# Performance work log

Measured on AMD Instinct MI355X. Metric: run time of the kernel, lower is better.

Reference implementation:

```python
import jax, jax.numpy as jnp
import numpy as np

N, K, DIM = 50000, 16, 256
SLOPE = 0.2

def _leaky(x):
    return jnp.where(x >= 0, x, SLOPE * x)

def _mlp(x, w, b):
    # torch nn.Linear followed by LeakyReLU(0.2); w is [in, out]
    return _leaky(x @ w + b)

def setup_inputs() -> dict:
    key = jax.random.key(0)
    ks = jax.random.split(key, 14)
    d4, d2 = DIM // 4, DIM // 2
    def lin(k, i, o):
        kw, kb = jax.random.split(k)
        s = 1.0 / np.sqrt(i)
        return (jax.random.uniform(kw, (i, o), jnp.float32, -s, s),
                jax.random.uniform(kb, (o,), jnp.float32, -s, s))
    w_res, b_res = lin(ks[0], DIM, DIM)
    w_init, b_init = lin(ks[1], DIM, d4)
    w_g1, b_g1 = lin(ks[2], 4, d4)
    w_g2, b_g2 = lin(ks[3], 4, d2)
    w_fin, b_fin = lin(ks[4], DIM, DIM)
    return {
        "input_features": jax.random.normal(ks[5], (N, DIM), jnp.float32),
        "geom_features": jax.random.normal(ks[6], (N, K, 4), jnp.float32),
        "closest_indices": jax.random.randint(ks[7], (N, K), 0, N, jnp.int32),
        "w_res": w_res, "b_res": b_res,
        "w_init": w_init, "b_init": b_init,
        "w_g1": w_g1, "b_g1": b_g1,
        "w_g2": w_g2, "b_g2": b_g2,
        "w_fin": w_fin, "b_fin": b_fin,
    }

def _lfa(feat, geom, idx, w_g, b_g):
    # feat: [N, d]; geom: [N, K, 4]; idx: [N, K]
    g = _mlp(geom, w_g, b_g)                 # [N, K, d]
    gathered = feat[idx]                      # [N, K, d] gather over points
    combined = jnp.concatenate([g, gathered], axis=-1)  # [N, K, 2d]
    return jnp.mean(combined, axis=1)         # [N, 2d]

def reference(input_features, geom_features, closest_indices,
              w_res, b_res, w_init, b_init, w_g1, b_g1, w_g2, b_g2,
              w_fin, b_fin):
    residual = _mlp(input_features, w_res, b_res)            # [N, DIM]
    a = _mlp(input_features, w_init, b_init)                 # [N, DIM/4]
    a = _lfa(a, geom_features, closest_indices, w_g1, b_g1)  # [N, DIM/2]
    a = _lfa(a, geom_features, closest_indices, w_g2, b_g2)  # [N, DIM]
    a = _mlp(a, w_fin, b_fin)                                # [N, DIM]
    return a + residual
```

## Files before the change

kernel.cpp:

```cpp
#include <hip/hip_runtime.h>

#define DIM 256
#define KNN 16
#define SLOPE 0.2f

typedef unsigned short u16;
typedef __attribute__((ext_vector_type(8))) unsigned short u16x8;
typedef __attribute__((ext_vector_type(4))) unsigned short u16x4;
typedef __attribute__((ext_vector_type(8))) short s16x8;
typedef __attribute__((ext_vector_type(4))) float f32x4;

__device__ __forceinline__ float leaky(float x) { return x >= 0.f ? x : SLOPE * x; }
__device__ __forceinline__ u16 f2bu(float f) {
    unsigned int u = __float_as_uint(f);
    u = (u + 0x7FFFu + ((u >> 16) & 1u)) >> 16;
    return (u16)u;
}
__device__ __forceinline__ float bu2f(u16 h) {
    return __uint_as_float(((unsigned int)h) << 16);
}

__global__ __launch_bounds__(256) void k_prep(
    const float* __restrict__ w_res, const float* __restrict__ w_init,
    const float* __restrict__ w_fin, u16* __restrict__ wT1, u16* __restrict__ wT3)
{
    const int t = blockIdx.x * 256 + threadIdx.x;
    if (t < 20 * 8 * 64) {
        const int lane = t & 63, frag = t >> 6;
        const int ks = frag & 7, ct = frag >> 3;
        const int col = ct * 16 + (lane & 15);
        const int k0 = ks * 32 + (lane >> 4) * 8;
        u16x8 p;
        #pragma unroll
        for (int j = 0; j < 8; ++j) {
            float v = (col < 256) ? w_res[(size_t)(k0 + j) * 256 + col]
                                  : w_init[(size_t)(k0 + j) * 64 + (col - 256)];
            p[j] = f2bu(v);
        }
        *(u16x8*)(wT1 + (size_t)t * 8) = p;
    } else if (t < 20 * 8 * 64 + 16 * 8 * 64) {
        const int u = t - 20 * 8 * 64;
        const int lane = u & 63, frag = u >> 6;
        const int ks = frag & 7, ct = frag >> 3;
        const int col = ct * 16 + (lane & 15);
        const int k0 = ks * 32 + (lane >> 4) * 8;
        u16x8 p;
        #pragma unroll
        for (int j = 0; j < 8; ++j)
            p[j] = f2bu(w_fin[(size_t)(k0 + j) * 256 + col]);
        *(u16x8*)(wT3 + (size_t)u * 8) = p;
    }
}

#define APAD 264
__global__ __launch_bounds__(256) void k_gemm1(
    const float* __restrict__ in, const u16* __restrict__ wT1,
    const float* __restrict__ b_res, const float* __restrict__ b_init,
    float* __restrict__ resid, u16* __restrict__ a1, int N)
{
    __shared__ u16 A_s[64 * APAD];
    const int t = threadIdx.x;
    const int base = blockIdx.x * 64;

    {
        const int row = t >> 2, seg = t & 3;
        const int grow = min(base + row, N - 1);
        const float* src = in + (size_t)grow * DIM + seg * 64;
        u16* dst = &A_s[row * APAD + seg * 64];
        #pragma unroll
        for (int j = 0; j < 8; ++j) {
            float4 f0 = *(const float4*)(src + j * 8);
            float4 f1 = *(const float4*)(src + j * 8 + 4);
            u16x8 p;
            p[0] = f2bu(f0.x); p[1] = f2bu(f0.y); p[2] = f2bu(f0.z); p[3] = f2bu(f0.w);
            p[4] = f2bu(f1.x); p[5] = f2bu(f1.y); p[6] = f2bu(f1.z); p[7] = f2bu(f1.w);
            *(u16x8*)(dst + j * 8) = p;
        }
    }
    __syncthreads();

    f32x4 acc[4][5];
    #pragma unroll
    for (int i = 0; i < 4; ++i)
        #pragma unroll
        for (int j = 0; j < 5; ++j)
            acc[i][j] = (f32x4){0.f, 0.f, 0.f, 0.f};

    const int w = t >> 6, lane = t & 63;
    const int llow = lane & 15, lhi = lane >> 4;

    for (int ks = 0; ks < 8; ++ks) {
        s16x8 bfrag[5];
        #pragma unroll
        for (int ci = 0; ci < 5; ++ci) {
            const int ct = w * 5 + ci;
            bfrag[ci] = *(const s16x8*)(wT1 + ((size_t)(ct * 8 + ks) * 64 + lane) * 8);
        }
        s16x8 afrag[4];
        #pragma unroll
        for (int rt = 0; rt < 4; ++rt)
            afrag[rt] = *(const s16x8*)(&A_s[(rt * 16 + llow) * APAD + ks * 32 + lhi * 8]);
        #pragma unroll
        for (int ci = 0; ci < 5; ++ci)
            #pragma unroll
            for (int rt = 0; rt < 4; ++rt)
                acc[rt][ci] = __builtin_amdgcn_mfma_f32_16x16x32_bf16(
                    afrag[rt], bfrag[ci], acc[rt][ci], 0, 0, 0);
    }

    #pragma unroll
    for (int ci = 0; ci < 5; ++ci) {
        const int ct = w * 5 + ci;
        const int col = ct * 16 + llow;
        if (col < 256) {
            const float bias = b_res[col];
            #pragma unroll
            for (int rt = 0; rt < 4; ++rt)
                #pragma unroll
                for (int r = 0; r < 4; ++r) {
                    int row = base + rt * 16 + lhi * 4 + r;
                    if (row < N)
                        resid[(size_t)row * DIM + col] = leaky(acc[rt][ci][r] + bias);
                }
        } else {
            const int c2 = col - 256;
            const float bias = b_init[c2];
            #pragma unroll
            for (int rt = 0; rt < 4; ++rt)
                #pragma unroll
                for (int r = 0; r < 4; ++r) {
                    int row = base + rt * 16 + lhi * 4 + r;
                    if (row < N)
                        a1[(size_t)row * 64 + c2] = f2bu(leaky(acc[rt][ci][r] + bias));
                }
        }
    }
}

__global__ __launch_bounds__(256) void k_lfa1(
    const float* __restrict__ geom, const int* __restrict__ idx,
    const float* __restrict__ w_g1, const float* __restrict__ b_g1,
    const u16* __restrict__ a1, u16* __restrict__ a2, int N)
{
    __shared__ float geom_s[16 * KNN * 4];
    __shared__ int idx_s[16 * KNN];
    const int t = threadIdx.x;
    const int base = blockIdx.x * 16;

    {
        size_t off = (size_t)base * 64 + t * 4;
        size_t mx = (size_t)N * 64 - 4;
        if (off > mx) off = mx;
        *(float4*)&geom_s[t * 4] = *(const float4*)(geom + off);
        int io = base * KNN + t;
        if (t < 256) idx_s[t] = idx[min(io, N * KNN - 1)];
    }
    __syncthreads();

    const int pt = t >> 4, s = t & 15;
    const int n = base + pt;

    float wr[4][4], bb[4];
    #pragma unroll
    for (int r = 0; r < 4; ++r)
        #pragma unroll
        for (int j = 0; j < 4; ++j)
            wr[r][j] = w_g1[r * 64 + s * 4 + j];
    #pragma unroll
    for (int j = 0; j < 4; ++j) bb[j] = b_g1[s * 4 + j];

    float accM[4] = {0.f, 0.f, 0.f, 0.f};
    const float4* g4 = (const float4*)&geom_s[pt * 64];
    #pragma unroll
    for (int k = 0; k < KNN; ++k) {
        float4 g = g4[k];
        #pragma unroll
        for (int j = 0; j < 4; ++j)
            accM[j] += leaky(g.x * wr[0][j] + g.y * wr[1][j] + g.z * wr[2][j] + g.w * wr[3][j] + bb[j]);
    }

    float accG[4] = {0.f, 0.f, 0.f, 0.f};
    #pragma unroll
    for (int k = 0; k < KNN; ++k) {
        u16x4 u = *(const u16x4*)(a1 + (size_t)idx_s[pt * KNN + k] * 64 + s * 4);
        #pragma unroll
        for (int j = 0; j < 4; ++j) accG[j] += bu2f(u[j]);
    }

    if (n < N) {
        u16x4 pm, pg;
        #pragma unroll
        for (int j = 0; j < 4; ++j) {
            pm[j] = f2bu(accM[j] * 0.0625f);
            pg[j] = f2bu(accG[j] * 0.0625f);
        }
        *(u16x4*)(a2 + (size_t)n * 128 + s * 4) = pm;
        *(u16x4*)(a2 + (size_t)n * 128 + 64 + s * 4) = pg;
    }
}

__global__ __launch_bounds__(256) void k_lfa2_fin(
    const float* __restrict__ geom, const int* __restrict__ idx,
    const float* __restrict__ w_g2, const float* __restrict__ b_g2,
    const u16* __restrict__ a2, const u16* __restrict__ wT3,
    const float* __restrict__ b_fin, float* __restrict__ out, int N)
{
    __shared__ u16 a3_s[64 * APAD];
    __shared__ float geom_s[64 * KNN * 4];
    __shared__ int idx_s[64 * KNN];
    const int t = threadIdx.x;
    const int base = blockIdx.x * 64;

    {
        size_t mx = (size_t)N * 64 - 4;
        #pragma unroll
        for (int j = 0; j < 4; ++j) {
            size_t off = (size_t)base * 64 + t * 4 + j * 1024;
            if (off > mx) off = mx;
            *(float4*)&geom_s[t * 4 + j * 1024] = *(const float4*)(geom + off);
        }
        int imx = N * KNN - 1;
        #pragma unroll
        for (int j = 0; j < 4; ++j) {
            int off = base * KNN + t + j * 256;
            idx_s[t + j * 256] = idx[min(off, imx)];
        }
    }
    __syncthreads();

    {
        const int c = t & 127, h = t >> 7;
        const float w0 = w_g2[c], w1 = w_g2[128 + c], w2 = w_g2[256 + c],
                    w3 = w_g2[384 + c], bb = b_g2[c];
        for (int p = 0; p < 32; ++p) {
            const int pt = h * 32 + p;
            float acc = 0.f;
            const float4* g4 = (const float4*)&geom_s[pt * 64];
            #pragma unroll
            for (int k = 0; k < KNN; ++k) {
                float4 g = g4[k];
                acc += leaky(g.x * w0 + g.y * w1 + g.z * w2 + g.w * w3 + bb);
            }
            a3_s[pt * APAD + c] = f2bu(acc * 0.0625f);
        }
    }
    {
        const int pt = t >> 2, q = t & 3;
        float acc[32];
        #pragma unroll
        for (int j = 0; j < 32; ++j) acc[j] = 0.f;
        for (int k = 0; k < KNN; ++k) {
            const u16* row = a2 + (size_t)idx_s[pt * KNN + k] * 128 + q * 32;
            #pragma unroll
            for (int v = 0; v < 4; ++v) {
                u16x8 u = *(const u16x8*)(row + v * 8);
                #pragma unroll
                for (int j = 0; j < 8; ++j) acc[v * 8 + j] += bu2f(u[j]);
            }
        }
        #pragma unroll
        for (int v = 0; v < 4; ++v) {
            u16x8 p;
            #pragma unroll
            for (int j = 0; j < 8; ++j) p[j] = f2bu(acc[v * 8 + j] * 0.0625f);
            *(u16x8*)(&a3_s[pt * APAD + 128 + q * 32 + v * 8]) = p;
        }
    }
    __syncthreads();

    f32x4 acc[4][4];
    #pragma unroll
    for (int i = 0; i < 4; ++i)
        #pragma unroll
        for (int j = 0; j < 4; ++j)
            acc[i][j] = (f32x4){0.f, 0.f, 0.f, 0.f};

    const int w = t >> 6, lane = t & 63;
    const int llow = lane & 15, lhi = lane >> 4;

    for (int ks = 0; ks < 8; ++ks) {
        s16x8 bfrag[4];
        #pragma unroll
        for (int ci = 0; ci < 4; ++ci) {
            const int ct = w * 4 + ci;
            bfrag[ci] = *(const s16x8*)(wT3 + ((size_t)(ct * 8 + ks) * 64 + lane) * 8);
        }
        s16x8 afrag[4];
        #pragma unroll
        for (int rt = 0; rt < 4; ++rt)
            afrag[rt] = *(const s16x8*)(&a3_s[(rt * 16 + llow) * APAD + ks * 32 + lhi * 8]);
        #pragma unroll
        for (int ci = 0; ci < 4; ++ci)
            #pragma unroll
            for (int rt = 0; rt < 4; ++rt)
                acc[rt][ci] = __builtin_amdgcn_mfma_f32_16x16x32_bf16(
                    afrag[rt], bfrag[ci], acc[rt][ci], 0, 0, 0);
    }

    #pragma unroll
    for (int ci = 0; ci < 4; ++ci) {
        const int ct = w * 4 + ci;
        const int col = ct * 16 + llow;
        const float bias = b_fin[col];
        #pragma unroll
        for (int rt = 0; rt < 4; ++rt)
            #pragma unroll
            for (int r = 0; r < 4; ++r) {
                int row = base + rt * 16 + lhi * 4 + r;
                if (row < N) {
                    size_t o = (size_t)row * DIM + col;
                    out[o] = leaky(acc[rt][ci][r] + bias) + out[o];
                }
            }
    }
}

extern "C" void kernel_launch(void* const* d_in, const int* in_sizes, int n_in,
                              void* d_out, int out_size, void* d_ws, size_t ws_size,
                              hipStream_t stream) {
    const float* in    = (const float*)d_in[0];
    const float* geom  = (const float*)d_in[1];
    const int*   idx   = (const int*)d_in[2];
    const float* w_res = (const float*)d_in[3];
    const float* b_res = (const float*)d_in[4];
    const float* w_init= (const float*)d_in[5];
    const float* b_init= (const float*)d_in[6];
    const float* w_g1  = (const float*)d_in[7];
    const float* b_g1  = (const float*)d_in[8];
    const float* w_g2  = (const float*)d_in[9];
    const float* b_g2  = (const float*)d_in[10];
    const float* w_fin = (const float*)d_in[11];
    const float* b_fin = (const float*)d_in[12];
    float* out = (float*)d_out;

    const int N = in_sizes[0] / DIM;

    char* ws = (char*)d_ws;
    u16* a1  = (u16*)ws;
    u16* a2  = (u16*)(ws + (size_t)N * 64 * 2);
    u16* wT1 = (u16*)(ws + (size_t)N * (64 + 128) * 2);
    u16* wT3 = wT1 + 320 * 256;

    k_prep<<<72, 256, 0, stream>>>(w_res, w_init, w_fin, wT1, wT3);
    k_gemm1<<<(N + 63) / 64, 256, 0, stream>>>(in, wT1, b_res, b_init, out, a1, N);
    k_lfa1<<<(N + 15) / 16, 256, 0, stream>>>(geom, idx, w_g1, b_g1, a1, a2, N);
    k_lfa2_fin<<<(N + 63) / 64, 256, 0, stream>>>(geom, idx, w_g2, b_g2, a2, wT3, b_fin, out, N);
}
```

Before: 296.9 us.

## Split second neighbor gather into column-sliced kernel with planar a2 layout

Stores the lfa1 output as eight 16-column planes, each 32 bytes per point, in place of 256-byte rows. A new kernel gathers one plane per block so the random neighbor reads for each slice hit a smaller working set, which can stay in L2/MALL. The final GEMM kernel then reads the precomputed gathered means. This adds a kernel launch and an extra round trip of the N×128 intermediate through global memory, and it drops the gather's overlap with the GEMM kernel.

```diff
diff --git a/kernel.cpp b/kernel.cpp
--- a/kernel.cpp
+++ b/kernel.cpp
@@ -53,6 +53,7 @@
 }
 
 #define APAD 264
+
 __global__ __launch_bounds__(256) void k_gemm1(
     const float* __restrict__ in, const u16* __restrict__ wT1,
     const float* __restrict__ b_res, const float* __restrict__ b_init,
@@ -140,7 +141,7 @@
 __global__ __launch_bounds__(256) void k_lfa1(
     const float* __restrict__ geom, const int* __restrict__ idx,
     const float* __restrict__ w_g1, const float* __restrict__ b_g1,
-    const u16* __restrict__ a1, u16* __restrict__ a2, int N)
+    const u16* __restrict__ a1, u16* __restrict__ a2g, int N)
 {
     __shared__ float geom_s[16 * KNN * 4];
     __shared__ int idx_s[16 * KNN];
@@ -194,20 +195,65 @@
             pm[j] = f2bu(accM[j] * 0.0625f);
             pg[j] = f2bu(accG[j] * 0.0625f);
         }
-        *(u16x4*)(a2 + (size_t)n * 128 + s * 4) = pm;
-        *(u16x4*)(a2 + (size_t)n * 128 + 64 + s * 4) = pg;
-    }
-}
-
-__global__ __launch_bounds__(256) void k_lfa2_fin(
-    const float* __restrict__ geom, const int* __restrict__ idx,
+        *(u16x4*)(a2g + ((size_t)(s >> 2) * N + n) * 16 + (s & 3) * 4) = pm;
+        *(u16x4*)(a2g + ((size_t)(4 + (s >> 2)) * N + n) * 16 + (s & 3) * 4) = pg;
+    }
+}
+
+__global__ __launch_bounds__(256) void k_gather2_cs(
+    const int* __restrict__ idx, const u16* __restrict__ a2g,
+    u16* __restrict__ a3g, int N)
+{
+    const int slice = blockIdx.x & 7;
+    const int n = (blockIdx.x >> 3) * 256 + threadIdx.x;
+    if (n >= N) return;
+    const u16* plane = a2g + (size_t)slice * N * 16;
+
+    int4 i0 = *(const int4*)(idx + (size_t)n * KNN);
+    int4 i1 = *(const int4*)(idx + (size_t)n * KNN + 4);
+    int4 i2 = *(const int4*)(idx + (size_t)n * KNN + 8);
+    int4 i3 = *(const int4*)(idx + (size_t)n * KNN + 12);
+    const int ind[16] = {i0.x, i0.y, i0.z, i0.w, i1.x, i1.y, i1.z, i1.w,
+                         i2.x, i2.y, i2.z, i2.w, i3.x, i3.y, i3.z, i3.w};
+
+    float acc[16];
+    #pragma unroll
+    for (int j = 0; j < 16; ++j) acc[j] = 0.f;
+
+    #pragma unroll
+    for (int k = 0; k < KNN; k += 2) {
+        const u16* r0 = plane + (size_t)ind[k] * 16;
+        const u16* r1 = plane + (size_t)ind[k + 1] * 16;
+        u16x8 u0a = *(const u16x8*)(r0);
+        u16x8 u0b = *(const u16x8*)(r0 + 8);
+        u16x8 u1a = *(const u16x8*)(r1);
+        u16x8 u1b = *(const u16x8*)(r1 + 8);
+        #pragma unroll
+        for (int j = 0; j < 8; ++j) {
+            acc[j]     += bu2f(u0a[j]) + bu2f(u1a[j]);
+            acc[j + 8] += bu2f(u0b[j]) + bu2f(u1b[j]);
+        }
+    }
+
+    u16x8 p0, p1;
+    #pragma unroll
+    for (int j = 0; j < 8; ++j) {
+        p0[j] = f2bu(acc[j] * 0.0625f);
+        p1[j] = f2bu(acc[j + 8] * 0.0625f);
+    }
+    u16* dst = a3g + ((size_t)slice * N + n) * 16;
+    *(u16x8*)(dst) = p0;
+    *(u16x8*)(dst + 8) = p1;
+}
+
+__global__ __launch_bounds__(256) void k_fin(
+    const float* __restrict__ geom, const u16* __restrict__ a3g,
     const float* __restrict__ w_g2, const float* __restrict__ b_g2,
-    const u16* __restrict__ a2, const u16* __restrict__ wT3,
-    const float* __restrict__ b_fin, float* __restrict__ out, int N)
+    const u16* __restrict__ wT3, const float* __restrict__ b_fin,
+    float* __restrict__ out, int N)
 {
     __shared__ u16 a3_s[64 * APAD];
     __shared__ float geom_s[64 * KNN * 4];
-    __shared__ int idx_s[64 * KNN];
     const int t = threadIdx.x;
     const int base = blockIdx.x * 64;
 
@@ -218,12 +264,6 @@
             size_t off = (size_t)base * 64 + t * 4 + j * 1024;
             if (off > mx) off = mx;
             *(float4*)&geom_s[t * 4 + j * 1024] = *(const float4*)(geom + off);
-        }
-        int imx = N * KNN - 1;
-        #pragma unroll
-        for (int j = 0; j < 4; ++j) {
-            int off = base * KNN + t + j * 256;
-            idx_s[t + j * 256] = idx[min(off, imx)];
         }
     }
     __syncthreads();
@@ -245,25 +285,16 @@
         }
     }
     {
-        const int pt = t >> 2, q = t & 3;
-        float acc[32];
-        #pragma unroll
-        for (int j = 0; j < 32; ++j) acc[j] = 0.f;
-        for (int k = 0; k < KNN; ++k) {
-            const u16* row = a2 + (size_t)idx_s[pt * KNN + k] * 128 + q * 32;
-            #pragma unroll
-            for (int v = 0; v < 4; ++v) {
-                u16x8 u = *(const u16x8*)(row + v * 8);
-                #pragma unroll
-                for (int j = 0; j < 8; ++j) acc[v * 8 + j] += bu2f(u[j]);
-            }
-        }
-        #pragma unroll
-        for (int v = 0; v < 4; ++v) {
-            u16x8 p;
-            #pragma unroll
-            for (int j = 0; j < 8; ++j) p[j] = f2bu(acc[v * 8 + j] * 0.0625f);
-            *(u16x8*)(&a3_s[pt * APAD + 128 + q * 32 + v * 8]) = p;
+        #pragma unroll
+        for (int j = 0; j < 2; ++j) {
+            const int id = t + 256 * j;
+            const int s = id >> 6, pt = id & 63;
+            const int row = min(base + pt, N - 1);
+            const u16* src = a3g + ((size_t)s * N + row) * 16;
+            u16x8 v0 = *(const u16x8*)(src);
+            u16x8 v1 = *(const u16x8*)(src + 8);
+            *(u16x8*)(&a3_s[pt * APAD + 128 + s * 16]) = v0;
+            *(u16x8*)(&a3_s[pt * APAD + 128 + s * 16 + 8]) = v1;
         }
     }
     __syncthreads();
@@ -337,12 +368,16 @@
 
     char* ws = (char*)d_ws;
     u16* a1  = (u16*)ws;
-    u16* a2  = (u16*)(ws + (size_t)N * 64 * 2);
-    u16* wT1 = (u16*)(ws + (size_t)N * (64 + 128) * 2);
+    u16* a2g = a1 + (size_t)N * 64;
+    u16* a3g = a2g + (size_t)N * 128;
+    u16* wT1 = a3g + (size_t)N * 128;
     u16* wT3 = wT1 + 320 * 256;
+
+    const int nchunk = (N + 255) / 256;
 
     k_prep<<<72, 256, 0, stream>>>(w_res, w_init, w_fin, wT1, wT3);
     k_gemm1<<<(N + 63) / 64, 256, 0, stream>>>(in, wT1, b_res, b_init, out, a1, N);
-    k_lfa1<<<(N + 15) / 16, 256, 0, stream>>>(geom, idx, w_g1, b_g1, a1, a2, N);
-    k_lfa2_fin<<<(N + 63) / 64, 256, 0, stream>>>(geom, idx, w_g2, b_g2, a2, wT3, b_fin, out, N);
-}
+    k_lfa1<<<(N + 15) / 16, 256, 0, stream>>>(geom, idx, w_g1, b_g1, a1, a2g, N);
+    k_gather2_cs<<<nchunk * 8, 256, 0, stream>>>(idx, a2g, a3g, N);
+    k_fin<<<(N + 63) / 64, 256, 0, stream>>>(geom, a3g, w_g2, b_g2, wT3, b_fin, out, N);
+}
```

Result: slower. 324.1 us (+9.2%).
